# Kernel tuning notes

Hardware: AMD Instinct MI355X
Metric: run time of the kernel (lower is better)

Reference implementation:

```python
import jax, jax.numpy as jnp
import numpy as np

IN, OUT, WS = 128, 64, 512
B, H, W = 4, 128, 128
GAIN = (2.0 / (1.0 + 0.2 ** 2)) ** 0.5  # util.lrelu_gain for leaky_relu(0.2)
EPS = 1e-8


def up2_bilinear_ac(x):
    # bilinear upsample x2, align_corners=True (torch F.upsample_bilinear semantics)
    _, _, h, w = x.shape
    ys = jnp.linspace(0.0, h - 1.0, 2 * h)
    xs = jnp.linspace(0.0, w - 1.0, 2 * w)
    y0 = jnp.floor(ys).astype(jnp.int32)
    y1 = jnp.minimum(y0 + 1, h - 1)
    wy = (ys - y0).astype(x.dtype)
    x0 = jnp.floor(xs).astype(jnp.int32)
    x1 = jnp.minimum(x0 + 1, w - 1)
    wx = (xs - x0).astype(x.dtype)
    t = x[:, :, y0, :] * (1 - wy)[None, None, :, None] + x[:, :, y1, :] * wy[None, None, :, None]
    return t[:, :, :, x0] * (1 - wx) + t[:, :, :, x1] * wx


def convt3(x, w):
    # torch conv_transpose2d(stride=1, padding=1, k=3) == conv2d with spatially
    # flipped kernel, weight layout [I,O,3,3] -> lax 'IOHW' spec, SAME padding.
    wf = w[:, :, ::-1, ::-1]
    return jax.lax.conv_general_dilated(
        x, wf, (1, 1), ((1, 1), (1, 1)),
        dimension_numbers=('NCHW', 'IOHW', 'NCHW'))


def mod_conv(x, style, w, he):
    # StyleGAN2 modulate + demodulate, expressed in fused activation form:
    # y[b,o] = demod[b,o] * convT(x[b] * style[b,:,None,None], he*W)  (same math
    # as building the per-sample grouped weight tensor in the original).
    wh = w * he                                  # [I,O,3,3]
    wsq = jnp.sum(wh * wh, axis=(2, 3))          # [I,O]
    d = jax.lax.rsqrt(jnp.einsum('bi,io->bo', style * style, wsq) + EPS)  # [B,O]
    y = convt3(x * style[:, :, None, None], wh)
    return y * d[:, :, None, None] * GAIN        # forward also multiplies by gain


def setup_inputs() -> dict:
    key = jax.random.key(0)
    ks = jax.random.split(key, 16)
    f = lambda k, s: jax.random.normal(k, s, dtype=jnp.float32)
    return {
        'x': f(ks[0], (B, IN, H, W)),
        'w': f(ks[1], (B, WS, 1, 1)),
        'conv1_w': f(ks[2], (IN, OUT, 3, 3)),
        'conv2_w': f(ks[3], (OUT, OUT, 3, 3)),
        'bias1': jnp.zeros((1, OUT, 1, 1), jnp.float32),
        'bias2': jnp.zeros((1, OUT, 1, 1), jnp.float32),
        'aaff1_w': f(ks[4], (IN, WS)),
        'aaff1_b': jnp.zeros((IN,), jnp.float32),
        'aaff2_w': f(ks[5], (OUT, WS)),
        'aaff2_b': jnp.zeros((OUT,), jnp.float32),
        'baff1_w': f(ks[6], (OUT,)) * 0.1,
        'baff2_w': f(ks[7], (OUT,)) * 0.1,
        'rgb_w': f(ks[8], (3, OUT)),
        'rgb_b': jnp.zeros((3,), jnp.float32),
        'noise1': f(ks[9], (B, 1, 2 * H, 2 * W)),
        'noise2': f(ks[10], (B, 1, 2 * H, 2 * W)),
    }


def reference(x, w, conv1_w, conv2_w, bias1, bias2, aaff1_w, aaff1_b,
              aaff2_w, aaff2_b, baff1_w, baff2_w, rgb_w, rgb_b,
              noise1, noise2):
    he1 = GAIN / (IN * 9) ** 0.5
    he2 = GAIN / (OUT * 9) ** 0.5
    he_a = 1.0 / WS ** 0.5
    he_rgb = 0.03 / OUT ** 0.5

    xu = up2_bilinear_ac(x)                       # [B,IN,2H,2W]
    wv = w[:, :, 0, 0]                            # [B,WS]

    s1 = jnp.einsum('ow,bw->bo', aaff1_w * he_a, wv) + aaff1_b
    h = mod_conv(xu, s1, conv1_w, he1)
    h = h + noise1 * baff1_w[None, :, None, None] + bias1
    h = jax.nn.leaky_relu(h, 0.2)

    s2 = jnp.einsum('ow,bw->bo', aaff2_w * he_a, wv) + aaff2_b
    h = mod_conv(h, s2, conv2_w, he2)
    h = h + noise2 * baff2_w[None, :, None, None] + bias2
    h = jax.nn.leaky_relu(h, 0.2)

    rgb = jnp.einsum('oc,bchw->bohw', rgb_w * he_rgb, h) + rgb_b[None, :, None, None]
    return (h, rgb)
```

## Files before the change

kernel.cpp:

```cpp
#include <hip/hip_runtime.h>
#include <hip/hip_bf16.h>
#include <math.h>

#define BN 4
#define CIN 128
#define COUT 64
#define WSDIM 512
#define HI 128
#define WI 128
#define HO 256
#define WO 256
#define EPSC 1e-8f
#define GAINC 1.3867504905630728f
#define HE1 (GAINC/33.941125496954285f)
#define HE2 (GAINC/24.0f)
#define SUP (127.0f/255.0f)

typedef __attribute__((ext_vector_type(8))) short s16x8;
typedef __attribute__((ext_vector_type(4))) float f32x4_t;
typedef __attribute__((ext_vector_type(4))) unsigned int u32x4;

static __device__ __forceinline__ float lrelu(float v){ return v > 0.f ? v : 0.2f*v; }
static __device__ __forceinline__ unsigned short bfbits(float v){
  __hip_bfloat16 h = __float2bfloat16(v);
  return *reinterpret_cast<unsigned short*>(&h);
}
static __device__ __forceinline__ unsigned int packbf(float a, float b){
  return (unsigned int)bfbits(a) | ((unsigned int)bfbits(b) << 16);
}

__global__ __launch_bounds__(256) void k_prep(
    const float* __restrict__ w, const float* __restrict__ c1w, const float* __restrict__ c2w,
    const float* __restrict__ a1w, const float* __restrict__ a1b,
    const float* __restrict__ a2w, const float* __restrict__ a2b,
    unsigned short* __restrict__ B1, unsigned short* __restrict__ B2,
    float* __restrict__ s1, float* __restrict__ s2,
    float* __restrict__ d1g, float* __restrict__ d2g)
{
  const int g = blockIdx.x, t = threadIdx.x;
  __shared__ float sh1[CIN];
  __shared__ float sh2[COUT];
  if (g < 144) {
    int cc = g / 36, r = g - cc * 36, k = r >> 2, ot = r & 3;
    for (int e = t; e < 512; e += 256) {
      int l = e >> 3, j = e & 7;
      int c = cc * 32 + (l >> 4) * 8 + j, o = ot * 16 + (l & 15);
      B1[g * 512 + e] = bfbits(c1w[(c * COUT + o) * 9 + (8 - k)] * HE1);
    }
  } else if (g < 288) {
    int g2 = g - 144;
    int cc = g2 / 36, r = g2 - cc * 36, k = r >> 2, ot = r & 3;
    for (int e = t; e < 512; e += 256) {
      int l = e >> 3, j = e & 7;
      int c = cc * 32 + (l >> 4) * 8 + j, o = ot * 16 + (l & 15);
      B2[g2 * 512 + e] = bfbits(c2w[(c * COUT + o) * 9 + (8 - k)] * HE2);
    }
  } else {
    const int b = g - 288;
    const float he_a = 0.044194173824159216f;
    const float* wv = w + b * WSDIM;
    if (t < CIN) {
      float acc = 0.f;
      const float* ap = a1w + t * WSDIM;
      for (int k = 0; k < WSDIM; ++k) acc += ap[k] * wv[k];
      float v = acc * he_a + a1b[t];
      sh1[t] = v; s1[b * CIN + t] = v;
    } else if (t < CIN + COUT) {
      int o = t - CIN;
      float acc = 0.f;
      const float* ap = a2w + o * WSDIM;
      for (int k = 0; k < WSDIM; ++k) acc += ap[k] * wv[k];
      float v = acc * he_a + a2b[o];
      sh2[o] = v; s2[b * COUT + o] = v;
    }
    __syncthreads();
    const int o = t >> 2, p = t & 3;
    float acc = 0.f;
    for (int c = p * 32; c < p * 32 + 32; ++c) {
      const float* wp = c1w + (size_t)(c * COUT + o) * 9;
      float ws_ = 0.f;
      #pragma unroll
      for (int k = 0; k < 9; ++k) ws_ += wp[k] * wp[k];
      acc += sh1[c] * sh1[c] * ws_;
    }
    acc += __shfl_xor(acc, 1); acc += __shfl_xor(acc, 2);
    if (p == 0) d1g[b * COUT + o] = rsqrtf(acc * HE1 * HE1 + EPSC) * GAINC;
    float ac2 = 0.f;
    for (int c = p * 16; c < p * 16 + 16; ++c) {
      const float* wp = c2w + (size_t)(c * COUT + o) * 9;
      float ws_ = 0.f;
      #pragma unroll
      for (int k = 0; k < 9; ++k) ws_ += wp[k] * wp[k];
      ac2 += sh2[c] * sh2[c] * ws_;
    }
    ac2 += __shfl_xor(ac2, 1); ac2 += __shfl_xor(ac2, 2);
    if (p == 0) d2g[b * COUT + o] = rsqrtf(ac2 * HE2 * HE2 + EPSC) * GAINC;
  }
}

__global__ __launch_bounds__(256) void k_conv1(
    const float* __restrict__ x, const unsigned short* __restrict__ B1pre,
    const float* __restrict__ s1, const float* __restrict__ noise1,
    const float* __restrict__ bias1, const float* __restrict__ baff1,
    const float* __restrict__ d1g, const float* __restrict__ s2,
    unsigned short* __restrict__ h1)
{
  const int id = blockIdx.x;
  const int swz = (id & 7) * 128 + (id >> 3);
  const int b = swz >> 8;
  const int oy0 = ((swz >> 4) & 15) * 16, ox0 = (swz & 15) * 16;
  const int tid = threadIdx.x;
  const int lane = tid & 63, wv = tid >> 6;
  const int lx = lane & 15, lg = lane >> 4;

  __shared__ __align__(16) float patch[11 * 12 * 36];
  __shared__ __align__(16) unsigned int ldsA[324 * 20];
  __shared__ float s1L[CIN];

  const int ty = oy0 > 0 ? oy0 - 1 : 0;
  const int tx = ox0 > 0 ? ox0 - 1 : 0;
  const int py0 = min((ty * 127) / 255, HI - 11);
  const int px0 = min((tx * 127) / 255, WI - 12);

  if (tid < CIN) s1L[tid] = s1[b * CIN + tid];

  f32x4_t acc[4][4];
  #pragma unroll
  for (int i = 0; i < 4; ++i)
    #pragma unroll
    for (int j = 0; j < 4; ++j) acc[i][j] = (f32x4_t){0.f, 0.f, 0.f, 0.f};

  float pr[5][4];
  auto PLOAD = [&](int cc) {
    #pragma unroll
    for (int i = 0; i < 5; ++i) {
      int u = tid + i * 256;
      if (u < 1056) {
        int pair = u / 3, part = u - pair * 3;
        int ch = pair & 31, r = pair >> 5;
        const float* src = x + (((size_t)b * CIN + cc * 32 + ch) << 14)
                             + (py0 + r) * WI + px0 + part * 4;
        pr[i][0] = src[0]; pr[i][1] = src[1]; pr[i][2] = src[2]; pr[i][3] = src[3];
      }
    }
  };
  auto PSTORE = [&]() {
    #pragma unroll
    for (int i = 0; i < 5; ++i) {
      int u = tid + i * 256;
      if (u < 1056) {
        int pair = u / 3, part = u - pair * 3;
        int ch = pair & 31, r = pair >> 5;
        float* dst = &patch[(r * 12 + part * 4) * 36 + ch];
        dst[0] = pr[i][0]; dst[36] = pr[i][1]; dst[72] = pr[i][2]; dst[108] = pr[i][3];
      }
    }
  };

  const s16x8* Bb = (const s16x8*)B1pre;

  PLOAD(0);
  for (int cc = 0; cc < 4; ++cc) {
    __syncthreads();
    PSTORE();
    __syncthreads();
    if (cc < 3) PLOAD(cc + 1);
    for (int e = tid; e < 1296; e += 256) {
      int pos = e >> 2, q = e & 3;
      int ys = pos / 18, xs = pos - ys * 18;
      int yy = oy0 - 1 + ys, xx = ox0 - 1 + xs;
      u32x4 outv = {0u, 0u, 0u, 0u};
      if (yy >= 0 && yy < HO && xx >= 0 && xx < WO) {
        float fy = yy * SUP; int y0 = (int)fy; float wy = fy - (float)y0;
        float fx = xx * SUP; int x0 = (int)fx; float wx = fx - (float)x0;
        int r0 = y0 - py0, r1 = min(y0 + 1, HI - 1) - py0;
        int c0 = x0 - px0, c1 = min(x0 + 1, WI - 1) - px0;
        const float* p00 = &patch[(r0 * 12 + c0) * 36 + q * 8];
        const float* p01 = &patch[(r0 * 12 + c1) * 36 + q * 8];
        const float* p10 = &patch[(r1 * 12 + c0) * 36 + q * 8];
        const float* p11 = &patch[(r1 * 12 + c1) * 36 + q * 8];
        unsigned int pk[4];
        #pragma unroll
        for (int h = 0; h < 2; ++h) {
          f32x4_t a00 = *(const f32x4_t*)(p00 + h * 4);
          f32x4_t a01 = *(const f32x4_t*)(p01 + h * 4);
          f32x4_t a10 = *(const f32x4_t*)(p10 + h * 4);
          f32x4_t a11 = *(const f32x4_t*)(p11 + h * 4);
          f32x4_t sv = *(const f32x4_t*)&s1L[cc * 32 + q * 8 + h * 4];
          float v[4];
          #pragma unroll
          for (int j = 0; j < 4; ++j) {
            float t0 = a00[j] + (a10[j] - a00[j]) * wy;
            float t1 = a01[j] + (a11[j] - a01[j]) * wy;
            v[j] = (t0 + (t1 - t0) * wx) * sv[j];
          }
          pk[h * 2 + 0] = packbf(v[0], v[1]);
          pk[h * 2 + 1] = packbf(v[2], v[3]);
        }
        outv = (u32x4){pk[0], pk[1], pk[2], pk[3]};
      }
      *(u32x4*)(ldsA + pos * 20 + q * 4) = outv;
    }
    __syncthreads();
    #pragma unroll
    for (int k = 0; k < 9; ++k) {
      const int dy = k / 3, dx = k - 3 * (k / 3);
      s16x8 b0 = Bb[((cc * 9 + k) * 4 + 0) * 64 + lane];
      s16x8 b1 = Bb[((cc * 9 + k) * 4 + 1) * 64 + lane];
      s16x8 b2 = Bb[((cc * 9 + k) * 4 + 2) * 64 + lane];
      s16x8 b3 = Bb[((cc * 9 + k) * 4 + 3) * 64 + lane];
      #pragma unroll
      for (int yi = 0; yi < 4; ++yi) {
        int row = (wv * 4 + yi + dy) * 18 + (lx + dx);
        s16x8 a = *(const s16x8*)((const char*)ldsA + (size_t)row * 80 + lg * 16);
        acc[yi][0] = __builtin_amdgcn_mfma_f32_16x16x32_bf16(a, b0, acc[yi][0], 0, 0, 0);
        acc[yi][1] = __builtin_amdgcn_mfma_f32_16x16x32_bf16(a, b1, acc[yi][1], 0, 0, 0);
        acc[yi][2] = __builtin_amdgcn_mfma_f32_16x16x32_bf16(a, b2, acc[yi][2], 0, 0, 0);
        acc[yi][3] = __builtin_amdgcn_mfma_f32_16x16x32_bf16(a, b3, acc[yi][3], 0, 0, 0);
      }
    }
  }
  #pragma unroll
  for (int yi = 0; yi < 4; ++yi) {
    int y = oy0 + wv * 4 + yi;
    f32x4_t nv = *(const f32x4_t*)(noise1 + (size_t)b * HO * WO + (size_t)y * WO + ox0 + lg * 4);
    #pragma unroll
    for (int ot = 0; ot < 4; ++ot) {
      int o = ot * 16 + lx;
      float d = d1g[b * COUT + o], ba = baff1[o], bi = bias1[o], sv = s2[b * COUT + o];
      #pragma unroll
      for (int jj = 0; jj < 4; ++jj) {
        float v = acc[yi][ot][jj] * d + nv[jj] * ba + bi;
        v = lrelu(v) * sv;
        int xg = ox0 + lg * 4 + jj;
        h1[(((size_t)b * HO + y) * WO + xg) * COUT + o] = bfbits(v);
      }
    }
  }
}

__global__ __launch_bounds__(256, 3) void k_conv2(
    const unsigned short* __restrict__ h1, const unsigned short* __restrict__ B2pre,
    const float* __restrict__ noise2, const float* __restrict__ bias2, const float* __restrict__ baff2,
    const float* __restrict__ d2g, const float* __restrict__ rgbw, const float* __restrict__ rgbb,
    float* __restrict__ hout, float* __restrict__ rgbout)
{
  const int id = blockIdx.x;
  const int swz = (id & 7) * 128 + (id >> 3);
  const int b = swz >> 8;
  const int oy0 = ((swz >> 4) & 15) * 16, ox0 = (swz & 15) * 16;
  const int tid = threadIdx.x;
  const int lane = tid & 63, wv = tid >> 6;
  const int lx = lane & 15, lg = lane >> 4;

  __shared__ unsigned int ldsA[2][324 * 20];

  f32x4_t acc[4][4];
  #pragma unroll
  for (int i = 0; i < 4; ++i)
    #pragma unroll
    for (int j = 0; j < 4; ++j) acc[i][j] = (f32x4_t){0.f, 0.f, 0.f, 0.f};

  const s16x8* Bb = (const s16x8*)B2pre;

  u32x4 rg[6];
  auto LOAD = [&](int cc) {
    #pragma unroll
    for (int i = 0; i < 6; ++i) {
      int e = i * 256 + tid;
      u32x4 v = {0, 0, 0, 0};
      if (e < 1296) {
        int pos = e >> 2, q = e & 3;
        int ys = pos / 18, xs = pos - ys * 18;
        int yy = oy0 - 1 + ys, xx = ox0 - 1 + xs;
        if (yy >= 0 && yy < HO && xx >= 0 && xx < WO)
          v = *(const u32x4*)(h1 + ((((size_t)b * HO + yy) * WO + xx) * COUT + cc * 32 + q * 8));
      }
      rg[i] = v;
    }
  };
  auto STORE = [&](unsigned int* buf) {
    #pragma unroll
    for (int i = 0; i < 6; ++i) {
      int e = i * 256 + tid;
      if (e < 1296) {
        int pos = e >> 2, q = e & 3;
        *(u32x4*)(buf + pos * 20 + q * 4) = rg[i];
      }
    }
  };

  LOAD(0);
  for (int cc = 0; cc < 2; ++cc) {
    if (cc) __syncthreads();
    STORE(&ldsA[cc & 1][0]);
    __syncthreads();
    if (cc < 1) LOAD(cc + 1);
    const unsigned int* buf = &ldsA[cc & 1][0];
    #pragma unroll
    for (int k = 0; k < 9; ++k) {
      const int dy = k / 3, dx = k - 3 * (k / 3);
      s16x8 b0 = Bb[((cc * 9 + k) * 4 + 0) * 64 + lane];
      s16x8 b1 = Bb[((cc * 9 + k) * 4 + 1) * 64 + lane];
      s16x8 b2 = Bb[((cc * 9 + k) * 4 + 2) * 64 + lane];
      s16x8 b3 = Bb[((cc * 9 + k) * 4 + 3) * 64 + lane];
      #pragma unroll
      for (int yi = 0; yi < 4; ++yi) {
        int row = (wv * 4 + yi + dy) * 18 + (lx + dx);
        s16x8 a = *(const s16x8*)((const char*)buf + (size_t)row * 80 + lg * 16);
        acc[yi][0] = __builtin_amdgcn_mfma_f32_16x16x32_bf16(a, b0, acc[yi][0], 0, 0, 0);
        acc[yi][1] = __builtin_amdgcn_mfma_f32_16x16x32_bf16(a, b1, acc[yi][1], 0, 0, 0);
        acc[yi][2] = __builtin_amdgcn_mfma_f32_16x16x32_bf16(a, b2, acc[yi][2], 0, 0, 0);
        acc[yi][3] = __builtin_amdgcn_mfma_f32_16x16x32_bf16(a, b3, acc[yi][3], 0, 0, 0);
      }
    }
  }
  const float her = 0.03f / 8.0f;
  #pragma unroll
  for (int yi = 0; yi < 4; ++yi) {
    int y = oy0 + wv * 4 + yi;
    f32x4_t nv = *(const f32x4_t*)(noise2 + (size_t)b * HO * WO + (size_t)y * WO + ox0 + lg * 4);
    float r[3][4];
    #pragma unroll
    for (int ch = 0; ch < 3; ++ch)
      #pragma unroll
      for (int jj = 0; jj < 4; ++jj) r[ch][jj] = 0.f;
    #pragma unroll
    for (int ot = 0; ot < 4; ++ot) {
      int o = ot * 16 + lx;
      float d = d2g[b * COUT + o], ba = baff2[o], bi = bias2[o];
      float w0 = rgbw[o], w1 = rgbw[COUT + o], w2 = rgbw[2 * COUT + o];
      f32x4_t hv;
      #pragma unroll
      for (int jj = 0; jj < 4; ++jj) {
        float v = acc[yi][ot][jj] * d + nv[jj] * ba + bi;
        v = lrelu(v);
        hv[jj] = v;
        r[0][jj] += w0 * v; r[1][jj] += w1 * v; r[2][jj] += w2 * v;
      }
      *(f32x4_t*)(hout + ((size_t)(b * COUT + o) * HO + y) * WO + ox0 + lg * 4) = hv;
    }
    #pragma unroll
    for (int ch = 0; ch < 3; ++ch)
      #pragma unroll
      for (int jj = 0; jj < 4; ++jj) {
        float s = r[ch][jj];
        s += __shfl_xor(s, 1); s += __shfl_xor(s, 2);
        s += __shfl_xor(s, 4); s += __shfl_xor(s, 8);
        r[ch][jj] = s;
      }
    if (lx < 12) {
      float val = 0.f;
      #pragma unroll
      for (int ii = 0; ii < 12; ++ii) if (lx == ii) val = r[ii >> 2][ii & 3];
      int ch = lx >> 2, jj = lx & 3;
      rgbout[(((size_t)(b * 3 + ch)) * HO + y) * WO + ox0 + lg * 4 + jj] = val * her + rgbb[ch];
    }
  }
}

extern "C" void kernel_launch(void* const* d_in, const int* in_sizes, int n_in,
                              void* d_out, int out_size, void* d_ws, size_t ws_size,
                              hipStream_t stream) {
  const float* x      = (const float*)d_in[0];
  const float* w      = (const float*)d_in[1];
  const float* c1w    = (const float*)d_in[2];
  const float* c2w    = (const float*)d_in[3];
  const float* bias1  = (const float*)d_in[4];
  const float* bias2  = (const float*)d_in[5];
  const float* a1w    = (const float*)d_in[6];
  const float* a1b    = (const float*)d_in[7];
  const float* a2w    = (const float*)d_in[8];
  const float* a2b    = (const float*)d_in[9];
  const float* baff1  = (const float*)d_in[10];
  const float* baff2  = (const float*)d_in[11];
  const float* rgbw   = (const float*)d_in[12];
  const float* rgbb   = (const float*)d_in[13];
  const float* noise1 = (const float*)d_in[14];
  const float* noise2 = (const float*)d_in[15];

  const size_t h1_bytes = (size_t)BN * HO * WO * COUT * 2;
  unsigned short* h1 = (unsigned short*)d_ws;
  char* p = (char*)d_ws + h1_bytes;
  float* s1  = (float*)p;               p += BN * CIN * 4;
  float* s2  = (float*)p;               p += BN * COUT * 4;
  float* d1g = (float*)p;               p += BN * COUT * 4;
  float* d2g = (float*)p;               p += BN * COUT * 4;
  unsigned short* B1pre = (unsigned short*)p;  p += 144 * 512 * 2;
  unsigned short* B2pre = (unsigned short*)p;

  float* hout   = (float*)d_out;
  float* rgbout = hout + (size_t)BN * COUT * HO * WO;

  k_prep<<<292, 256, 0, stream>>>(w, c1w, c2w, a1w, a1b, a2w, a2b, B1pre, B2pre, s1, s2, d1g, d2g);
  k_conv1<<<1024, 256, 0, stream>>>(x, B1pre, s1, noise1, bias1, baff1, d1g, s2, h1);
  k_conv2<<<1024, 256, 0, stream>>>(h1, B2pre, noise2, bias2, baff2, d2g, rgbw, rgbb, hout, rgbout);
}
```

Measured before the change: 142.5 us.

## Load conv2 halo tiles directly global-to-LDS and fold style into patch staging

In conv2, the register-staged halo load and store with double buffering is replaced by direct global_load_lds 16-byte transfers of both channel chunks up front. Out-of-bounds lanes read from a zeroed page written by the prep kernel, and there is a single barrier before the MFMA loop. The LDS row stride shrinks from 80 to 64 bytes in both convs, which removes the padding and may add bank conflicts on the A-fragment reads. Conv1 now applies the style scale once per source pixel during patch staging instead of per bilinear output, and the conv2 occupancy hint of 3 is dropped.

```diff
diff --git a/kernel.cpp b/kernel.cpp
--- a/kernel.cpp
+++ b/kernel.cpp
@@ -28,6 +28,11 @@
 static __device__ __forceinline__ unsigned int packbf(float a, float b){
   return (unsigned int)bfbits(a) | ((unsigned int)bfbits(b) << 16);
 }
+static __device__ __forceinline__ void gload_lds16(const void* g, void* l){
+  __builtin_amdgcn_global_load_lds(
+      (const __attribute__((address_space(1))) void*)g,
+      (__attribute__((address_space(3))) void*)l, 16, 0, 0);
+}
 
 __global__ __launch_bounds__(256) void k_prep(
     const float* __restrict__ w, const float* __restrict__ c1w, const float* __restrict__ c2w,
@@ -35,12 +40,14 @@
     const float* __restrict__ a2w, const float* __restrict__ a2b,
     unsigned short* __restrict__ B1, unsigned short* __restrict__ B2,
     float* __restrict__ s1, float* __restrict__ s2,
-    float* __restrict__ d1g, float* __restrict__ d2g)
+    float* __restrict__ d1g, float* __restrict__ d2g,
+    unsigned int* __restrict__ zpage)
 {
   const int g = blockIdx.x, t = threadIdx.x;
   __shared__ float sh1[CIN];
   __shared__ float sh2[COUT];
   if (g < 144) {
+    if (g == 0 && t < 64) zpage[t] = 0u;
     int cc = g / 36, r = g - cc * 36, k = r >> 2, ot = r & 3;
     for (int e = t; e < 512; e += 256) {
       int l = e >> 3, j = e & 7;
@@ -114,7 +121,7 @@
   const int lx = lane & 15, lg = lane >> 4;
 
   __shared__ __align__(16) float patch[11 * 12 * 36];
-  __shared__ __align__(16) unsigned int ldsA[324 * 20];
+  __shared__ __align__(16) unsigned int ldsA[324 * 16];
   __shared__ float s1L[CIN];
 
   const int ty = oy0 > 0 ? oy0 - 1 : 0;
@@ -144,15 +151,17 @@
       }
     }
   };
-  auto PSTORE = [&]() {
+  auto PSTORE = [&](int cc) {
     #pragma unroll
     for (int i = 0; i < 5; ++i) {
       int u = tid + i * 256;
       if (u < 1056) {
         int pair = u / 3, part = u - pair * 3;
         int ch = pair & 31, r = pair >> 5;
+        float sv = s1L[cc * 32 + ch];
         float* dst = &patch[(r * 12 + part * 4) * 36 + ch];
-        dst[0] = pr[i][0]; dst[36] = pr[i][1]; dst[72] = pr[i][2]; dst[108] = pr[i][3];
+        dst[0] = pr[i][0] * sv; dst[36] = pr[i][1] * sv;
+        dst[72] = pr[i][2] * sv; dst[108] = pr[i][3] * sv;
       }
     }
   };
@@ -162,7 +171,7 @@
   PLOAD(0);
   for (int cc = 0; cc < 4; ++cc) {
     __syncthreads();
-    PSTORE();
+    PSTORE(cc);
     __syncthreads();
     if (cc < 3) PLOAD(cc + 1);
     for (int e = tid; e < 1296; e += 256) {
@@ -186,20 +195,19 @@
           f32x4_t a01 = *(const f32x4_t*)(p01 + h * 4);
           f32x4_t a10 = *(const f32x4_t*)(p10 + h * 4);
           f32x4_t a11 = *(const f32x4_t*)(p11 + h * 4);
-          f32x4_t sv = *(const f32x4_t*)&s1L[cc * 32 + q * 8 + h * 4];
           float v[4];
           #pragma unroll
           for (int j = 0; j < 4; ++j) {
             float t0 = a00[j] + (a10[j] - a00[j]) * wy;
             float t1 = a01[j] + (a11[j] - a01[j]) * wy;
-            v[j] = (t0 + (t1 - t0) * wx) * sv[j];
+            v[j] = t0 + (t1 - t0) * wx;
           }
           pk[h * 2 + 0] = packbf(v[0], v[1]);
           pk[h * 2 + 1] = packbf(v[2], v[3]);
         }
         outv = (u32x4){pk[0], pk[1], pk[2], pk[3]};
       }
-      *(u32x4*)(ldsA + pos * 20 + q * 4) = outv;
+      *(u32x4*)(ldsA + pos * 16 + q * 4) = outv;
     }
     __syncthreads();
     #pragma unroll
@@ -212,7 +220,7 @@
       #pragma unroll
       for (int yi = 0; yi < 4; ++yi) {
         int row = (wv * 4 + yi + dy) * 18 + (lx + dx);
-        s16x8 a = *(const s16x8*)((const char*)ldsA + (size_t)row * 80 + lg * 16);
+        s16x8 a = *(const s16x8*)((const char*)ldsA + (size_t)row * 64 + lg * 16);
         acc[yi][0] = __builtin_amdgcn_mfma_f32_16x16x32_bf16(a, b0, acc[yi][0], 0, 0, 0);
         acc[yi][1] = __builtin_amdgcn_mfma_f32_16x16x32_bf16(a, b1, acc[yi][1], 0, 0, 0);
         acc[yi][2] = __builtin_amdgcn_mfma_f32_16x16x32_bf16(a, b2, acc[yi][2], 0, 0, 0);
@@ -239,10 +247,11 @@
   }
 }
 
-__global__ __launch_bounds__(256, 3) void k_conv2(
+__global__ __launch_bounds__(256) void k_conv2(
     const unsigned short* __restrict__ h1, const unsigned short* __restrict__ B2pre,
     const float* __restrict__ noise2, const float* __restrict__ bias2, const float* __restrict__ baff2,
     const float* __restrict__ d2g, const float* __restrict__ rgbw, const float* __restrict__ rgbb,
+    const unsigned int* __restrict__ zpage,
     float* __restrict__ hout, float* __restrict__ rgbout)
 {
   const int id = blockIdx.x;
@@ -253,7 +262,7 @@
   const int lane = tid & 63, wv = tid >> 6;
   const int lx = lane & 15, lg = lane >> 4;
 
-  __shared__ unsigned int ldsA[2][324 * 20];
+  __shared__ __align__(16) unsigned int ldsA[2][1536 * 4];
 
   f32x4_t acc[4][4];
   #pragma unroll
@@ -263,40 +272,28 @@
 
   const s16x8* Bb = (const s16x8*)B2pre;
 
-  u32x4 rg[6];
-  auto LOAD = [&](int cc) {
+  const int e0u = __builtin_amdgcn_readfirstlane(tid & ~63);
+  #pragma unroll
+  for (int cc = 0; cc < 2; ++cc) {
     #pragma unroll
     for (int i = 0; i < 6; ++i) {
-      int e = i * 256 + tid;
-      u32x4 v = {0, 0, 0, 0};
-      if (e < 1296) {
-        int pos = e >> 2, q = e & 3;
-        int ys = pos / 18, xs = pos - ys * 18;
-        int yy = oy0 - 1 + ys, xx = ox0 - 1 + xs;
-        if (yy >= 0 && yy < HO && xx >= 0 && xx < WO)
-          v = *(const u32x4*)(h1 + ((((size_t)b * HO + yy) * WO + xx) * COUT + cc * 32 + q * 8));
-      }
-      rg[i] = v;
-    }
-  };
-  auto STORE = [&](unsigned int* buf) {
-    #pragma unroll
-    for (int i = 0; i < 6; ++i) {
-      int e = i * 256 + tid;
-      if (e < 1296) {
-        int pos = e >> 2, q = e & 3;
-        *(u32x4*)(buf + pos * 20 + q * 4) = rg[i];
-      }
-    }
-  };
-
-  LOAD(0);
+      int ebase = i * 256 + e0u;
+      int e = ebase + lane;
+      int pos = e >> 2, q = e & 3;
+      int ys = pos / 18, xs = pos - ys * 18;
+      int yy = oy0 - 1 + ys, xx = ox0 - 1 + xs;
+      bool ok = (e < 1296) && (yy >= 0) && (yy < HO) && (xx >= 0) && (xx < WO);
+      const void* src = ok
+          ? (const void*)(h1 + ((((size_t)b * HO + yy) * WO + xx) * COUT) + cc * 32 + q * 8)
+          : (const void*)zpage;
+      gload_lds16(src, (void*)&ldsA[cc][(size_t)ebase * 4]);
+    }
+  }
+  __syncthreads();
+
+  #pragma unroll
   for (int cc = 0; cc < 2; ++cc) {
-    if (cc) __syncthreads();
-    STORE(&ldsA[cc & 1][0]);
-    __syncthreads();
-    if (cc < 1) LOAD(cc + 1);
-    const unsigned int* buf = &ldsA[cc & 1][0];
+    const char* bufc = (const char*)ldsA[cc];
     #pragma unroll
     for (int k = 0; k < 9; ++k) {
       const int dy = k / 3, dx = k - 3 * (k / 3);
@@ -307,7 +304,7 @@
       #pragma unroll
       for (int yi = 0; yi < 4; ++yi) {
         int row = (wv * 4 + yi + dy) * 18 + (lx + dx);
-        s16x8 a = *(const s16x8*)((const char*)buf + (size_t)row * 80 + lg * 16);
+        s16x8 a = *(const s16x8*)(bufc + (size_t)row * 64 + lg * 16);
         acc[yi][0] = __builtin_amdgcn_mfma_f32_16x16x32_bf16(a, b0, acc[yi][0], 0, 0, 0);
         acc[yi][1] = __builtin_amdgcn_mfma_f32_16x16x32_bf16(a, b1, acc[yi][1], 0, 0, 0);
         acc[yi][2] = __builtin_amdgcn_mfma_f32_16x16x32_bf16(a, b2, acc[yi][2], 0, 0, 0);
@@ -387,12 +384,13 @@
   float* d1g = (float*)p;               p += BN * COUT * 4;
   float* d2g = (float*)p;               p += BN * COUT * 4;
   unsigned short* B1pre = (unsigned short*)p;  p += 144 * 512 * 2;
-  unsigned short* B2pre = (unsigned short*)p;
+  unsigned short* B2pre = (unsigned short*)p;  p += 144 * 512 * 2;
+  unsigned int* zpage = (unsigned int*)p;
 
   float* hout   = (float*)d_out;
   float* rgbout = hout + (size_t)BN * COUT * HO * WO;
 
-  k_prep<<<292, 256, 0, stream>>>(w, c1w, c2w, a1w, a1b, a2w, a2b, B1pre, B2pre, s1, s2, d1g, d2g);
+  k_prep<<<292, 256, 0, stream>>>(w, c1w, c2w, a1w, a1b, a2w, a2b, B1pre, B2pre, s1, s2, d1g, d2g, zpage);
   k_conv1<<<1024, 256, 0, stream>>>(x, B1pre, s1, noise1, bias1, baff1, d1g, s2, h1);
-  k_conv2<<<1024, 256, 0, stream>>>(h1, B2pre, noise2, bias2, baff2, d2g, rgbw, rgbb, hout, rgbout);
-}
+  k_conv2<<<1024, 256, 0, stream>>>(h1, B2pre, noise2, bias2, baff2, d2g, rgbw, rgbb, zpage, hout, rgbout);
+}
```

Measured after the change: 138.7 us. 2.7% less time.
